# Performance work log

Measured on AMD Instinct MI355X. Metric: run time of the kernel, lower is better.

Reference implementation:

```python
import jax, jax.numpy as jnp
import numpy as np
import math

B, S, D, H = 2, 2048, 512, 8
DK = D // H


def setup_inputs() -> dict:
    key = jax.random.key(0)
    ks = jax.random.split(key, 8)
    scale = 1.0 / math.sqrt(D)
    inp = {
        "query": jax.random.normal(ks[0], (B, S, D), dtype=jnp.float32),
        "key": jax.random.normal(ks[1], (B, S, D), dtype=jnp.float32),
        "value": jax.random.normal(ks[2], (B, S, D), dtype=jnp.float32),
        # causal mask, broadcast over batch and heads; masked_fill where mask == 0
        "mask": jnp.tril(jnp.ones((S, S), dtype=jnp.int32))[None, None, :, :],
        # nn.Linear(d_model, d_model, bias=False) weights, shape [out, in]
        "Wq": jax.random.uniform(ks[3], (D, D), jnp.float32, -scale, scale),
        "Wk": jax.random.uniform(ks[4], (D, D), jnp.float32, -scale, scale),
        "Wv": jax.random.uniform(ks[5], (D, D), jnp.float32, -scale, scale),
        "Wo": jax.random.uniform(ks[6], (D, D), jnp.float32, -scale, scale),
    }
    return inp


def reference(query, key, value, mask, Wq, Wk, Wv, Wo):
    b, s, d = query.shape
    h, dk = H, d // H
    q = query @ Wq.T                      # [B,S,D]
    _k_dead = key @ Wk.T                  # computed then discarded by the repo bug
    v = value @ Wv.T                      # [B,S,D]
    # raw .view() head split (NOT transpose-based) — faithful to the source
    qh = q.reshape(b, h, s, dk)           # [B,H,S,dk]
    kh = qh                               # repo bug: key = query.view(...)
    vh = v.reshape(b, h, s, dk)
    scores = jnp.einsum("bhqd,bhkd->bhqk", qh, kh) / math.sqrt(dk)  # [B,H,S,S]
    scores = jnp.where(mask == 0, jnp.float32(-1e9), scores)
    attn = jax.nn.softmax(scores, axis=-1)  # dropout p=0.0 -> identity
    x = jnp.einsum("bhqk,bhkd->bhqd", attn, vh)  # [B,H,S,dk]
    x = x.transpose(0, 2, 1, 3).reshape(b, s, h * dk)  # [B,S,D]
    return x @ Wo.T
```

## Files before the change

kernel.cpp:

```cpp
#include <hip/hip_runtime.h>


typedef unsigned short u16;
typedef unsigned int   u32;
typedef __attribute__((ext_vector_type(4))) float f32x4;
typedef __attribute__((ext_vector_type(8))) short bf16x8;
typedef __attribute__((ext_vector_type(4))) u16   us4;
typedef __attribute__((ext_vector_type(8))) u16   us8;

#define DEV static __device__ __forceinline__

DEV u16 f2b(float x) {
  union { float f; u32 u; } a; a.f = x;
  u32 u = a.u;
  u += 0x7fffu + ((u >> 16) & 1u);
  return (u16)(u >> 16);
}
DEV float b2f(u16 x) { union { u32 u; float f; } a; a.u = (u32)x << 16; return a.f; }
DEV us4 f4tob(f32x4 v) {
  us4 r; r[0] = f2b(v[0]); r[1] = f2b(v[1]); r[2] = f2b(v[2]); r[3] = f2b(v[3]);
  return r;
}

DEV u32 cvtpk(float lo, float hi) {
  u32 d;
  asm("v_cvt_pk_bf16_f32 %0, %1, %2" : "=v"(d) : "v"(lo), "v"(hi));
  return d;
}
DEV void swap32(u32& a, u32& b) {
  asm("v_permlane32_swap_b32 %0, %1" : "+v"(a), "+v"(b));
}
DEV void swap16(u32& a, u32& b) {
  asm("v_permlane16_swap_b32 %0, %1" : "+v"(a), "+v"(b));
}
DEV void swap32f(float& a, float& b) {
  asm("v_permlane32_swap_b32 %0, %1" : "+v"(a), "+v"(b));
}
DEV void swap16f(float& a, float& b) {
  asm("v_permlane16_swap_b32 %0, %1" : "+v"(a), "+v"(b));
}

DEV void gload16(const u16* g, u16* l) {
  __builtin_amdgcn_global_load_lds(
      (const __attribute__((address_space(1))) void*)(const void*)g,
      (__attribute__((address_space(3))) void*)(void*)l, 16, 0, 0);
}

__global__ __launch_bounds__(256)
void cvt_kernel(const float* __restrict__ q, const float* __restrict__ v,
                const float* __restrict__ wq, const float* __restrict__ wv,
                const float* __restrict__ wo,
                u16* __restrict__ aq, u16* __restrict__ av,
                u16* __restrict__ bq, u16* __restrict__ bv, u16* __restrict__ bo) {
  int cid = blockIdx.x * 256 + threadIdx.x;
  const float* src; u16* dst; int off;
  if      (cid < 262144) { src = q;  dst = aq; off = cid; }
  else if (cid < 524288) { src = v;  dst = av; off = cid - 262144; }
  else if (cid < 557056) { src = wq; dst = bq; off = cid - 524288; }
  else if (cid < 589824) { src = wv; dst = bv; off = cid - 557056; }
  else                   { src = wo; dst = bo; off = cid - 589824; }
  f32x4 a = *reinterpret_cast<const f32x4*>(src + (size_t)off * 8);
  f32x4 b = *reinterpret_cast<const f32x4*>(src + (size_t)off * 8 + 4);
  us4 lo = f4tob(a), hi = f4tob(b);
  us8 o;
  o[0] = lo[0]; o[1] = lo[1]; o[2] = lo[2]; o[3] = lo[3];
  o[4] = hi[0]; o[5] = hi[1]; o[6] = hi[2]; o[7] = hi[3];
  *reinterpret_cast<us8*>(dst + (size_t)off * 8) = o;
}

template<int EPI>
DEV void gemm_fast_body(const u16* __restrict__ A, const u16* __restrict__ Bw,
                        void* __restrict__ outp, int bm, int bn,
                        u16* __restrict__ sA, u16* __restrict__ sB) {
  const int tid  = threadIdx.x;
  const int lane = tid & 63;
  const int w    = tid >> 6;
  const int row0 = bm * 64, col0 = bn * 64;
  const int l16 = lane & 15, lhi = lane >> 4;
  const int wr = (w >> 1) * 32, wc = (w & 1) * 32;

  f32x4 acc[2][2];
#pragma unroll
  for (int mf = 0; mf < 2; ++mf)
#pragma unroll
    for (int nf = 0; nf < 2; ++nf) acc[mf][nf] = (f32x4)0.f;

  auto stage = [&](int buf, int kt) {
#pragma unroll
    for (int i = 0; i < 2; ++i) {
      int u0 = w * 128 + i * 64;
      int u  = u0 + lane;
      int r  = u >> 3;
      int s  = (u & 7) ^ (r & 7);
      gload16(A  + (size_t)(row0 + r) * 512 + kt + s * 8, &sA[buf * 4096 + u0 * 8]);
      gload16(Bw + (size_t)(col0 + r) * 512 + kt + s * 8, &sB[buf * 4096 + u0 * 8]);
    }
  };

  stage(0, 0);
  for (int t = 0; t < 8; ++t) {
    __syncthreads();
    if (t + 1 < 8) stage((t + 1) & 1, (t + 1) * 64);
    const u16* Ka = &sA[(t & 1) * 4096];
    const u16* Kb = &sB[(t & 1) * 4096];
    __builtin_amdgcn_s_setprio(1);
#pragma unroll
    for (int ks = 0; ks < 2; ++ks) {
      bf16x8 af[2], bv[2];
#pragma unroll
      for (int mf = 0; mf < 2; ++mf) {
        int unit = (ks * 4 + lhi) ^ (l16 & 7);
        af[mf] = *reinterpret_cast<const bf16x8*>(&Ka[(wr + mf * 16 + l16) * 64 + unit * 8]);
      }
#pragma unroll
      for (int nf = 0; nf < 2; ++nf) {
        int unit = (ks * 4 + lhi) ^ (l16 & 7);
        bv[nf] = *reinterpret_cast<const bf16x8*>(&Kb[(wc + nf * 16 + l16) * 64 + unit * 8]);
      }
#pragma unroll
      for (int mf = 0; mf < 2; ++mf)
#pragma unroll
        for (int nf = 0; nf < 2; ++nf)
          acc[mf][nf] = __builtin_amdgcn_mfma_f32_16x16x32_bf16(af[mf], bv[nf], acc[mf][nf], 0, 0, 0);
    }
    __builtin_amdgcn_s_setprio(0);
  }

#pragma unroll
  for (int mf = 0; mf < 2; ++mf)
#pragma unroll
    for (int nf = 0; nf < 2; ++nf)
#pragma unroll
      for (int r = 0; r < 4; ++r) {
        int grow = row0 + wr + mf * 16 + lhi * 4 + r;
        int gcol = col0 + wc + nf * 16 + l16;
        float v = acc[mf][nf][r];
        if constexpr (EPI == 0) {
          ((u16*)outp)[(size_t)grow * 512 + gcol] = f2b(v);
        } else if constexpr (EPI == 1) {
          int b = grow >> 11, srow = grow & 2047;
          int h = srow >> 8;
          int ss = ((srow & 255) << 3) + (gcol >> 6);
          int dd = gcol & 63;
          ((u16*)outp)[(((size_t)(b * 8 + h) * 64 + dd) << 11) + ss] = f2b(v);
        } else {
          ((float*)outp)[(size_t)grow * 512 + gcol] = v;
        }
      }
}

__global__ __launch_bounds__(256)
void qv_gemm_kernel(const u16* __restrict__ aq, const u16* __restrict__ av,
                    const u16* __restrict__ wqb, const u16* __restrict__ wvb,
                    u16* __restrict__ qbf, u16* __restrict__ vt) {
  __shared__ u16 sA[2 * 4096];
  __shared__ u16 sB[2 * 4096];
  const int xcd = blockIdx.x & 7;
  const int local = blockIdx.x >> 3;
  const int g = local >> 6, rem = local & 63;
  const int bm = xcd * 8 + (rem >> 3), bn = rem & 7;
  if (g == 0) gemm_fast_body<0>(aq, wqb, qbf, bm, bn, sA, sB);
  else        gemm_fast_body<1>(av, wvb, vt,  bm, bn, sA, sB);
}

__global__ __launch_bounds__(256)
void o_gemm_kernel(const u16* __restrict__ opre, const u16* __restrict__ wob,
                   float* __restrict__ out) {
  __shared__ u16 sA[2 * 4096];
  __shared__ u16 sB[2 * 4096];
  const int xcd = blockIdx.x & 7;
  const int local = blockIdx.x >> 3;
  const int bm = xcd * 8 + (local >> 3), bn = local & 7;
  gemm_fast_body<2>(opre, wob, out, bm, bn, sA, sB);
}

constexpr float SCL = 0.125f * 1.44269504088896340736f;
constexpr int NSPLIT = 4;

__global__ __launch_bounds__(256)
void attn_kernel(const u16* __restrict__ qbf, const u16* __restrict__ vt,
                 u16* __restrict__ opart, float* __restrict__ lsum) {
  __shared__ u16 sK[2][4096];
  __shared__ u16 sV[2][4096];
  const int tid  = threadIdx.x;
  const int lane = tid & 63;
  const int w    = tid >> 6;
  const int xcd  = blockIdx.x & 7;
  const int i    = blockIdx.x >> 3;
  const int qb   = 31 - (i >> 3);
  const int r8   = i & 7;
  const int bh   = 2 * xcd + (r8 >> 2);
  const int split = r8 & 3;
  const int q0 = qb * 64 + w * 16;
  const int l16 = lane & 15, lhi = lane >> 4;

  const u16* Qh = qbf + (size_t)bh * (2048 * 64);
  const u16* Vh = vt  + (size_t)bh * (64 * 2048);

  bf16x8 qf[2];
#pragma unroll
  for (int ks = 0; ks < 2; ++ks) {
    union { bf16x8 v; u32 wd[4]; } qw;
    qw.v = *reinterpret_cast<const bf16x8*>(&Qh[(q0 + l16) * 64 + ks * 32 + lhi * 8]);
#pragma unroll
    for (int j = 0; j < 4; ++j) {
      u32 u = qw.wd[j];
      float lo = b2f((u16)(u & 0xffffu)) * SCL;
      float hi = b2f((u16)(u >> 16)) * SCL;
      qw.wd[j] = cvtpk(lo, hi);
    }
    qf[ks] = qw.v;
  }

  f32x4 Oa[4];
#pragma unroll
  for (int nf = 0; nf < 4; ++nf) Oa[nf] = (f32x4)0.f;
  float rs = 0.f;

  const int ntiles = qb + 1;
  const int base = ntiles >> 2, rem = ntiles & 3;
  const int t0 = split * base + (split < rem ? split : rem);
  const int t1 = t0 + base + (split < rem ? 1 : 0);

  auto stage = [&](int buf, int t) {
    const int kb = t * 64;
#pragma unroll
    for (int j = 0; j < 2; ++j) {
      int u0 = w * 128 + j * 64;
      int u  = u0 + lane;
      int r  = u >> 3;
      int s  = (u & 7) ^ (r & 7);
      gload16(Qh + (size_t)(kb + r) * 64 + s * 8, &sK[buf][u0 * 8]);
      gload16(Vh + (size_t)r * 2048 + kb + s * 8, &sV[buf][u0 * 8]);
    }
  };

  if (t0 < t1) {
    stage(t0 & 1, t0);
    for (int kt = t0; kt < t1; ++kt) {
      __syncthreads();
      if (kt + 1 < t1) stage((kt + 1) & 1, kt + 1);
      const int kb = kt * 64;
      const u16* Kl = sK[kt & 1];
      const u16* Vl = sV[kt & 1];
      bf16x8 kf[8], vf[8];
#pragma unroll
      for (int nf = 0; nf < 4; ++nf)
#pragma unroll
        for (int ks = 0; ks < 2; ++ks) {
          int off = (nf * 16 + l16) * 64 + (((ks * 4 + lhi) ^ (l16 & 7)) * 8);
          kf[nf * 2 + ks] = *reinterpret_cast<const bf16x8*>(&Kl[off]);
          vf[nf * 2 + ks] = *reinterpret_cast<const bf16x8*>(&Vl[off]);
        }
      f32x4 s[4];
#pragma unroll
      for (int nf = 0; nf < 4; ++nf) s[nf] = (f32x4)0.f;
      __builtin_amdgcn_s_setprio(1);
#pragma unroll
      for (int nf = 0; nf < 4; ++nf)
#pragma unroll
        for (int ks = 0; ks < 2; ++ks)
          s[nf] = __builtin_amdgcn_mfma_f32_16x16x32_bf16(kf[nf * 2 + ks], qf[ks], s[nf], 0, 0, 0);
      __builtin_amdgcn_s_setprio(0);
      if (kb + 63 > q0) {
        const int row = q0 + l16;
#pragma unroll
        for (int nf = 0; nf < 4; ++nf)
#pragma unroll
          for (int r = 0; r < 4; ++r) {
            int col = kb + nf * 16 + lhi * 4 + r;
            if (col > row) s[nf][r] = -1e30f;
          }
      }
#pragma unroll
      for (int nf = 0; nf < 4; ++nf)
#pragma unroll
        for (int r = 0; r < 4; ++r) {
          float p = exp2f(s[nf][r]);
          s[nf][r] = p;
          rs += p;
        }
      u32 pk[4][2];
#pragma unroll
      for (int nf = 0; nf < 4; ++nf)
#pragma unroll
        for (int rr = 0; rr < 2; ++rr)
          pk[nf][rr] = cvtpk(s[nf][2 * rr], s[nf][2 * rr + 1]);
      union { u32 wd[4]; bf16x8 v; } pa[2];
#pragma unroll
      for (int ks = 0; ks < 2; ++ks)
#pragma unroll
        for (int rr = 0; rr < 2; ++rr) {
          u32 X = pk[2 * ks][rr], Y = pk[2 * ks + 1][rr];
          swap32(X, Y);
          swap16(X, Y);
          pa[ks].wd[rr]     = X;
          pa[ks].wd[2 + rr] = Y;
        }
      __builtin_amdgcn_s_setprio(1);
#pragma unroll
      for (int nf = 0; nf < 4; ++nf)
#pragma unroll
        for (int ks = 0; ks < 2; ++ks)
          Oa[nf] = __builtin_amdgcn_mfma_f32_16x16x32_bf16(pa[ks].v, vf[nf * 2 + ks], Oa[nf], 0, 0, 0);
      __builtin_amdgcn_s_setprio(0);
    }
  }

  {
    float a = rs, b = rs;
    swap16f(a, b);
    float y = a + b;
    float c = y, d = y;
    swap32f(c, d);
    rs = c + d;
  }

  u16* op = opart + ((size_t)split * 32768 + bh * 2048) * 64;
#pragma unroll
  for (int nf = 0; nf < 4; ++nf)
#pragma unroll
    for (int r = 0; r < 4; ++r) {
      int row = q0 + lhi * 4 + r;
      op[(size_t)row * 64 + nf * 16 + l16] = f2b(Oa[nf][r]);
    }
  if (lane < 16)
    lsum[(size_t)split * 32768 + bh * 2048 + q0 + lane] = rs;
}

__global__ __launch_bounds__(256)
void merge_kernel(const u16* __restrict__ opart, const float* __restrict__ lsum,
                  u16* __restrict__ opre) {
  const int gid = blockIdx.x * 256 + threadIdx.x;
  const int row = gid >> 3;
  const int c   = gid & 7;
  float den = 0.f;
#pragma unroll
  for (int s = 0; s < NSPLIT; ++s) den += lsum[(size_t)s * 32768 + row];
  const float inv = 1.f / den;
  float acc[8];
#pragma unroll
  for (int j = 0; j < 8; ++j) acc[j] = 0.f;
#pragma unroll
  for (int s = 0; s < NSPLIT; ++s) {
    us8 o = *reinterpret_cast<const us8*>(&opart[((size_t)s * 32768 + row) * 64 + c * 8]);
#pragma unroll
    for (int j = 0; j < 8; ++j) acc[j] += b2f(o[j]);
  }
  us8 o;
#pragma unroll
  for (int j = 0; j < 8; ++j) o[j] = f2b(acc[j] * inv);
  const int bh = row >> 11, srow = row & 2047;
  const int b = bh >> 3, h = bh & 7;
  *reinterpret_cast<us8*>(&opre[((size_t)b * 2048 + srow) * 512 + h * 64 + c * 8]) = o;
}

extern "C" void kernel_launch(void* const* d_in, const int* in_sizes, int n_in,
                              void* d_out, int out_size, void* d_ws, size_t ws_size,
                              hipStream_t stream) {
  const float* query = (const float*)d_in[0];
  const float* value = (const float*)d_in[2];
  const float* Wq = (const float*)d_in[4];
  const float* Wv = (const float*)d_in[6];
  const float* Wo = (const float*)d_in[7];

  u16* qbf   = (u16*)d_ws;
  u16* vt    = qbf + 2097152;
  u16* opre  = vt + 2097152;
  u16* opart = opre + 2097152;
  u16* aq    = opart + NSPLIT * 2097152;
  u16* av    = aq + 2097152;
  u16* wqb   = av + 2097152;
  u16* wvb   = wqb + 262144;
  u16* wob   = wvb + 262144;
  float* lsum = (float*)(wob + 262144);
  float* out = (float*)d_out;

  cvt_kernel<<<dim3(2432), dim3(256), 0, stream>>>(query, value, Wq, Wv, Wo,
                                                   aq, av, wqb, wvb, wob);
  qv_gemm_kernel<<<dim3(1024), dim3(256), 0, stream>>>(aq, av, wqb, wvb, qbf, vt);
  attn_kernel<<<dim3(2048), dim3(256), 0, stream>>>(qbf, vt, opart, lsum);
  merge_kernel<<<dim3(1024), dim3(256), 0, stream>>>(opart, lsum, opre);
  o_gemm_kernel<<<dim3(512), dim3(256), 0, stream>>>(opre, wob, out);
}
```

Before: 60.81 us.

## Fuse fp32-to-bf16 activation conversion into QV GEMM and split-merge into O GEMM

The standalone conversion of query/value to bf16 is removed. The QV GEMM now loads fp32 activations into registers, converts them and writes swizzled bf16 tiles to LDS, double-buffered around the MFMA loop. The merge kernel is also folded into the output-projection GEMM, which sums the four split partials, normalizes by the summed lsum and writes the A tile directly. This drops two launches and the bf16 intermediate round-trips. In exchange, A loads become register-staged instead of async global-to-LDS and need extra VALU work per tile.

```diff
diff --git a/kernel.cpp b/kernel.cpp
--- a/kernel.cpp
+++ b/kernel.cpp
@@ -47,18 +47,14 @@
 }
 
 __global__ __launch_bounds__(256)
-void cvt_kernel(const float* __restrict__ q, const float* __restrict__ v,
-                const float* __restrict__ wq, const float* __restrict__ wv,
-                const float* __restrict__ wo,
-                u16* __restrict__ aq, u16* __restrict__ av,
-                u16* __restrict__ bq, u16* __restrict__ bv, u16* __restrict__ bo) {
+void cvtw_kernel(const float* __restrict__ wq, const float* __restrict__ wv,
+                 const float* __restrict__ wo,
+                 u16* __restrict__ bq, u16* __restrict__ bv, u16* __restrict__ bo) {
   int cid = blockIdx.x * 256 + threadIdx.x;
   const float* src; u16* dst; int off;
-  if      (cid < 262144) { src = q;  dst = aq; off = cid; }
-  else if (cid < 524288) { src = v;  dst = av; off = cid - 262144; }
-  else if (cid < 557056) { src = wq; dst = bq; off = cid - 524288; }
-  else if (cid < 589824) { src = wv; dst = bv; off = cid - 557056; }
-  else                   { src = wo; dst = bo; off = cid - 589824; }
+  if      (cid < 32768) { src = wq; dst = bq; off = cid; }
+  else if (cid < 65536) { src = wv; dst = bv; off = cid - 32768; }
+  else                  { src = wo; dst = bo; off = cid - 65536; }
   f32x4 a = *reinterpret_cast<const f32x4*>(src + (size_t)off * 8);
   f32x4 b = *reinterpret_cast<const f32x4*>(src + (size_t)off * 8 + 4);
   us4 lo = f4tob(a), hi = f4tob(b);
@@ -68,64 +64,21 @@
   *reinterpret_cast<us8*>(dst + (size_t)off * 8) = o;
 }
 
+DEV void ds_writeA(u16* sA, int buf, int tid, const u32 w0[8]) {
+  union { u32 wd[4]; us8 v; } o0, o1;
+#pragma unroll
+  for (int j = 0; j < 4; ++j) { o0.wd[j] = w0[j]; o1.wd[j] = w0[4 + j]; }
+  int u0 = 2 * tid;
+  int r  = u0 >> 3;
+  int s0 = (u0 & 7) ^ (r & 7);
+  int s1 = ((u0 + 1) & 7) ^ (r & 7);
+  *reinterpret_cast<us8*>(&sA[buf * 4096 + r * 64 + s0 * 8]) = o0.v;
+  *reinterpret_cast<us8*>(&sA[buf * 4096 + r * 64 + s1 * 8]) = o1.v;
+}
+
 template<int EPI>
-DEV void gemm_fast_body(const u16* __restrict__ A, const u16* __restrict__ Bw,
-                        void* __restrict__ outp, int bm, int bn,
-                        u16* __restrict__ sA, u16* __restrict__ sB) {
-  const int tid  = threadIdx.x;
-  const int lane = tid & 63;
-  const int w    = tid >> 6;
-  const int row0 = bm * 64, col0 = bn * 64;
-  const int l16 = lane & 15, lhi = lane >> 4;
-  const int wr = (w >> 1) * 32, wc = (w & 1) * 32;
-
-  f32x4 acc[2][2];
-#pragma unroll
-  for (int mf = 0; mf < 2; ++mf)
-#pragma unroll
-    for (int nf = 0; nf < 2; ++nf) acc[mf][nf] = (f32x4)0.f;
-
-  auto stage = [&](int buf, int kt) {
-#pragma unroll
-    for (int i = 0; i < 2; ++i) {
-      int u0 = w * 128 + i * 64;
-      int u  = u0 + lane;
-      int r  = u >> 3;
-      int s  = (u & 7) ^ (r & 7);
-      gload16(A  + (size_t)(row0 + r) * 512 + kt + s * 8, &sA[buf * 4096 + u0 * 8]);
-      gload16(Bw + (size_t)(col0 + r) * 512 + kt + s * 8, &sB[buf * 4096 + u0 * 8]);
-    }
-  };
-
-  stage(0, 0);
-  for (int t = 0; t < 8; ++t) {
-    __syncthreads();
-    if (t + 1 < 8) stage((t + 1) & 1, (t + 1) * 64);
-    const u16* Ka = &sA[(t & 1) * 4096];
-    const u16* Kb = &sB[(t & 1) * 4096];
-    __builtin_amdgcn_s_setprio(1);
-#pragma unroll
-    for (int ks = 0; ks < 2; ++ks) {
-      bf16x8 af[2], bv[2];
-#pragma unroll
-      for (int mf = 0; mf < 2; ++mf) {
-        int unit = (ks * 4 + lhi) ^ (l16 & 7);
-        af[mf] = *reinterpret_cast<const bf16x8*>(&Ka[(wr + mf * 16 + l16) * 64 + unit * 8]);
-      }
-#pragma unroll
-      for (int nf = 0; nf < 2; ++nf) {
-        int unit = (ks * 4 + lhi) ^ (l16 & 7);
-        bv[nf] = *reinterpret_cast<const bf16x8*>(&Kb[(wc + nf * 16 + l16) * 64 + unit * 8]);
-      }
-#pragma unroll
-      for (int mf = 0; mf < 2; ++mf)
-#pragma unroll
-        for (int nf = 0; nf < 2; ++nf)
-          acc[mf][nf] = __builtin_amdgcn_mfma_f32_16x16x32_bf16(af[mf], bv[nf], acc[mf][nf], 0, 0, 0);
-    }
-    __builtin_amdgcn_s_setprio(0);
-  }
-
+DEV void gemm_epilogue(void* outp, int row0, int col0, int wr, int wc,
+                       int l16, int lhi, const f32x4 acc[2][2]) {
 #pragma unroll
   for (int mf = 0; mf < 2; ++mf)
 #pragma unroll
@@ -149,8 +102,82 @@
       }
 }
 
+template<int EPI>
+DEV void gemm_f32A_body(const float* __restrict__ Af, const u16* __restrict__ Bw,
+                        void* __restrict__ outp, int bm, int bn,
+                        u16* __restrict__ sA, u16* __restrict__ sB) {
+  const int tid  = threadIdx.x;
+  const int lane = tid & 63;
+  const int w    = tid >> 6;
+  const int row0 = bm * 64, col0 = bn * 64;
+  const int l16 = lane & 15, lhi = lane >> 4;
+  const int wr = (w >> 1) * 32, wc = (w & 1) * 32;
+  const int arow = tid >> 2, acol = (tid & 3) * 16;
+
+  f32x4 acc[2][2];
+#pragma unroll
+  for (int mf = 0; mf < 2; ++mf)
+#pragma unroll
+    for (int nf = 0; nf < 2; ++nf) acc[mf][nf] = (f32x4)0.f;
+
+  f32x4 ar[4];
+  auto loadA = [&](int kt) {
+    const float* src = &Af[(size_t)(row0 + arow) * 512 + kt + acol];
+#pragma unroll
+    for (int j = 0; j < 4; ++j) ar[j] = *reinterpret_cast<const f32x4*>(src + j * 4);
+  };
+  auto writeA = [&](int buf) {
+    u32 wds[8];
+#pragma unroll
+    for (int j = 0; j < 4; ++j) {
+      wds[2 * j]     = cvtpk(ar[j][0], ar[j][1]);
+      wds[2 * j + 1] = cvtpk(ar[j][2], ar[j][3]);
+    }
+    u32 ord[8] = {wds[0], wds[1], wds[2], wds[3], wds[4], wds[5], wds[6], wds[7]};
+    ds_writeA(sA, buf, tid, ord);
+  };
+  auto stageB = [&](int buf, int kt) {
+#pragma unroll
+    for (int i = 0; i < 2; ++i) {
+      int u0 = w * 128 + i * 64;
+      int u  = u0 + lane;
+      int r  = u >> 3;
+      int s  = (u & 7) ^ (r & 7);
+      gload16(Bw + (size_t)(col0 + r) * 512 + kt + s * 8, &sB[buf * 4096 + u0 * 8]);
+    }
+  };
+
+  loadA(0); stageB(0, 0); writeA(0);
+  for (int t = 0; t < 8; ++t) {
+    __syncthreads();
+    if (t + 1 < 8) { stageB((t + 1) & 1, (t + 1) * 64); loadA((t + 1) * 64); }
+    const u16* Ka = &sA[(t & 1) * 4096];
+    const u16* Kb = &sB[(t & 1) * 4096];
+    __builtin_amdgcn_s_setprio(1);
+#pragma unroll
+    for (int ks = 0; ks < 2; ++ks) {
+      bf16x8 af[2], bv[2];
+      int unit = (ks * 4 + lhi) ^ (l16 & 7);
+#pragma unroll
+      for (int mf = 0; mf < 2; ++mf)
+        af[mf] = *reinterpret_cast<const bf16x8*>(&Ka[(wr + mf * 16 + l16) * 64 + unit * 8]);
+#pragma unroll
+      for (int nf = 0; nf < 2; ++nf)
+        bv[nf] = *reinterpret_cast<const bf16x8*>(&Kb[(wc + nf * 16 + l16) * 64 + unit * 8]);
+#pragma unroll
+      for (int mf = 0; mf < 2; ++mf)
+#pragma unroll
+        for (int nf = 0; nf < 2; ++nf)
+          acc[mf][nf] = __builtin_amdgcn_mfma_f32_16x16x32_bf16(af[mf], bv[nf], acc[mf][nf], 0, 0, 0);
+    }
+    __builtin_amdgcn_s_setprio(0);
+    if (t + 1 < 8) writeA((t + 1) & 1);
+  }
+  gemm_epilogue<EPI>(outp, row0, col0, wr, wc, l16, lhi, acc);
+}
+
 __global__ __launch_bounds__(256)
-void qv_gemm_kernel(const u16* __restrict__ aq, const u16* __restrict__ av,
+void qv_gemm_kernel(const float* __restrict__ query, const float* __restrict__ value,
                     const u16* __restrict__ wqb, const u16* __restrict__ wvb,
                     u16* __restrict__ qbf, u16* __restrict__ vt) {
   __shared__ u16 sA[2 * 4096];
@@ -159,23 +186,107 @@
   const int local = blockIdx.x >> 3;
   const int g = local >> 6, rem = local & 63;
   const int bm = xcd * 8 + (rem >> 3), bn = rem & 7;
-  if (g == 0) gemm_fast_body<0>(aq, wqb, qbf, bm, bn, sA, sB);
-  else        gemm_fast_body<1>(av, wvb, vt,  bm, bn, sA, sB);
-}
+  if (g == 0) gemm_f32A_body<0>(query, wqb, qbf, bm, bn, sA, sB);
+  else        gemm_f32A_body<1>(value, wvb, vt,  bm, bn, sA, sB);
+}
+
+constexpr int NSPLIT = 4;
 
 __global__ __launch_bounds__(256)
-void o_gemm_kernel(const u16* __restrict__ opre, const u16* __restrict__ wob,
-                   float* __restrict__ out) {
+void o_gemm_kernel(const u16* __restrict__ opart, const float* __restrict__ lsum,
+                   const u16* __restrict__ wob, float* __restrict__ out) {
   __shared__ u16 sA[2 * 4096];
   __shared__ u16 sB[2 * 4096];
+  const int tid  = threadIdx.x;
+  const int lane = tid & 63;
+  const int w    = tid >> 6;
   const int xcd = blockIdx.x & 7;
   const int local = blockIdx.x >> 3;
   const int bm = xcd * 8 + (local >> 3), bn = local & 7;
-  gemm_fast_body<2>(opre, wob, out, bm, bn, sA, sB);
+  const int row0 = bm * 64, col0 = bn * 64;
+  const int l16 = lane & 15, lhi = lane >> 4;
+  const int wr = (w >> 1) * 32, wc = (w & 1) * 32;
+  const int arow = tid >> 2, acol = (tid & 3) * 16;
+  const int bb = bm >> 5;
+  const int srow = ((bm & 31) << 6) + arow;
+
+  f32x4 acc[2][2];
+#pragma unroll
+  for (int mf = 0; mf < 2; ++mf)
+#pragma unroll
+    for (int nf = 0; nf < 2; ++nf) acc[mf][nf] = (f32x4)0.f;
+
+  us8   po[NSPLIT][2];
+  float dens[NSPLIT];
+  auto loadA = [&](int t) {
+    size_t rb = (size_t)(bb * 8 + t) * 2048 + srow;
+#pragma unroll
+    for (int s = 0; s < NSPLIT; ++s) {
+      dens[s] = lsum[(size_t)s * 32768 + rb];
+      const u16* src = &opart[((size_t)s * 32768 + rb) * 64 + acol];
+      po[s][0] = *reinterpret_cast<const us8*>(src);
+      po[s][1] = *reinterpret_cast<const us8*>(src + 8);
+    }
+  };
+  auto writeA = [&](int buf) {
+    float inv = 1.f / (dens[0] + dens[1] + dens[2] + dens[3]);
+    float a[16];
+#pragma unroll
+    for (int j = 0; j < 8; ++j) {
+      float x0 = 0.f, x1 = 0.f;
+#pragma unroll
+      for (int s = 0; s < NSPLIT; ++s) {
+        x0 += b2f((u16)po[s][0][j]);
+        x1 += b2f((u16)po[s][1][j]);
+      }
+      a[j] = x0 * inv; a[8 + j] = x1 * inv;
+    }
+    u32 ord[8];
+#pragma unroll
+    for (int j = 0; j < 8; ++j) ord[j] = cvtpk(a[2 * j], a[2 * j + 1]);
+    ds_writeA(sA, buf, tid, ord);
+  };
+  auto stageB = [&](int buf, int kt) {
+#pragma unroll
+    for (int i = 0; i < 2; ++i) {
+      int u0 = w * 128 + i * 64;
+      int u  = u0 + lane;
+      int r  = u >> 3;
+      int s  = (u & 7) ^ (r & 7);
+      gload16(wob + (size_t)(col0 + r) * 512 + kt + s * 8, &sB[buf * 4096 + u0 * 8]);
+    }
+  };
+
+  loadA(0); stageB(0, 0); writeA(0);
+  for (int t = 0; t < 8; ++t) {
+    __syncthreads();
+    if (t + 1 < 8) { stageB((t + 1) & 1, (t + 1) * 64); loadA(t + 1); }
+    const u16* Ka = &sA[(t & 1) * 4096];
+    const u16* Kb = &sB[(t & 1) * 4096];
+    __builtin_amdgcn_s_setprio(1);
+#pragma unroll
+    for (int ks = 0; ks < 2; ++ks) {
+      bf16x8 af[2], bv[2];
+      int unit = (ks * 4 + lhi) ^ (l16 & 7);
+#pragma unroll
+      for (int mf = 0; mf < 2; ++mf)
+        af[mf] = *reinterpret_cast<const bf16x8*>(&Ka[(wr + mf * 16 + l16) * 64 + unit * 8]);
+#pragma unroll
+      for (int nf = 0; nf < 2; ++nf)
+        bv[nf] = *reinterpret_cast<const bf16x8*>(&Kb[(wc + nf * 16 + l16) * 64 + unit * 8]);
+#pragma unroll
+      for (int mf = 0; mf < 2; ++mf)
+#pragma unroll
+        for (int nf = 0; nf < 2; ++nf)
+          acc[mf][nf] = __builtin_amdgcn_mfma_f32_16x16x32_bf16(af[mf], bv[nf], acc[mf][nf], 0, 0, 0);
+    }
+    __builtin_amdgcn_s_setprio(0);
+    if (t + 1 < 8) writeA((t + 1) & 1);
+  }
+  gemm_epilogue<2>(out, row0, col0, wr, wc, l16, lhi, acc);
 }
 
 constexpr float SCL = 0.125f * 1.44269504088896340736f;
-constexpr int NSPLIT = 4;
 
 __global__ __launch_bounds__(256)
 void attn_kernel(const u16* __restrict__ qbf, const u16* __restrict__ vt,
@@ -328,33 +439,6 @@
     lsum[(size_t)split * 32768 + bh * 2048 + q0 + lane] = rs;
 }
 
-__global__ __launch_bounds__(256)
-void merge_kernel(const u16* __restrict__ opart, const float* __restrict__ lsum,
-                  u16* __restrict__ opre) {
-  const int gid = blockIdx.x * 256 + threadIdx.x;
-  const int row = gid >> 3;
-  const int c   = gid & 7;
-  float den = 0.f;
-#pragma unroll
-  for (int s = 0; s < NSPLIT; ++s) den += lsum[(size_t)s * 32768 + row];
-  const float inv = 1.f / den;
-  float acc[8];
-#pragma unroll
-  for (int j = 0; j < 8; ++j) acc[j] = 0.f;
-#pragma unroll
-  for (int s = 0; s < NSPLIT; ++s) {
-    us8 o = *reinterpret_cast<const us8*>(&opart[((size_t)s * 32768 + row) * 64 + c * 8]);
-#pragma unroll
-    for (int j = 0; j < 8; ++j) acc[j] += b2f(o[j]);
-  }
-  us8 o;
-#pragma unroll
-  for (int j = 0; j < 8; ++j) o[j] = f2b(acc[j] * inv);
-  const int bh = row >> 11, srow = row & 2047;
-  const int b = bh >> 3, h = bh & 7;
-  *reinterpret_cast<us8*>(&opre[((size_t)b * 2048 + srow) * 512 + h * 64 + c * 8]) = o;
-}
-
 extern "C" void kernel_launch(void* const* d_in, const int* in_sizes, int n_in,
                               void* d_out, int out_size, void* d_ws, size_t ws_size,
                               hipStream_t stream) {
@@ -366,20 +450,15 @@
 
   u16* qbf   = (u16*)d_ws;
   u16* vt    = qbf + 2097152;
-  u16* opre  = vt + 2097152;
-  u16* opart = opre + 2097152;
-  u16* aq    = opart + NSPLIT * 2097152;
-  u16* av    = aq + 2097152;
-  u16* wqb   = av + 2097152;
+  u16* opart = vt + 2097152;
+  u16* wqb   = opart + NSPLIT * 2097152;
   u16* wvb   = wqb + 262144;
   u16* wob   = wvb + 262144;
   float* lsum = (float*)(wob + 262144);
   float* out = (float*)d_out;
 
-  cvt_kernel<<<dim3(2432), dim3(256), 0, stream>>>(query, value, Wq, Wv, Wo,
-                                                   aq, av, wqb, wvb, wob);
-  qv_gemm_kernel<<<dim3(1024), dim3(256), 0, stream>>>(aq, av, wqb, wvb, qbf, vt);
+  cvtw_kernel<<<dim3(384), dim3(256), 0, stream>>>(Wq, Wv, Wo, wqb, wvb, wob);
+  qv_gemm_kernel<<<dim3(1024), dim3(256), 0, stream>>>(query, value, wqb, wvb, qbf, vt);
   attn_kernel<<<dim3(2048), dim3(256), 0, stream>>>(qbf, vt, opart, lsum);
-  merge_kernel<<<dim3(1024), dim3(256), 0, stream>>>(opart, lsum, opre);
-  o_gemm_kernel<<<dim3(512), dim3(256), 0, stream>>>(opre, wob, out);
-}
+  o_gemm_kernel<<<dim3(512), dim3(256), 0, stream>>>(opart, lsum, wob, out);
+}
```

Result: slower. 67.16 us, median of 3 (+10.4%).

## Use 128x128 tiles with triple-buffered pipeline in QV projection GEMM

Applied to the files above, without the earlier changes.

The Q/V projection GEMM moves from 64x64 tiles to 128x128 tiles, so each warp computes a 64x64 sub-tile with 16 MFMA accumulators. The grid shrinks from 1024 to 256 blocks. A three-stage LDS ring with two tiles in flight and explicit vmcnt waits replaces the double buffer. The aim is more data reuse per LDS load and better hiding of global-load latency. The trade-off is more registers and LDS per block, and only 256 blocks, which may leave compute units underused on a 256-CU part.

```diff
diff --git a/kernel.cpp b/kernel.cpp
--- a/kernel.cpp
+++ b/kernel.cpp
@@ -68,13 +68,111 @@
   *reinterpret_cast<us8*>(dst + (size_t)off * 8) = o;
 }
 
-template<int EPI>
-DEV void gemm_fast_body(const u16* __restrict__ A, const u16* __restrict__ Bw,
-                        void* __restrict__ outp, int bm, int bn,
-                        u16* __restrict__ sA, u16* __restrict__ sB) {
+__global__ __launch_bounds__(256)
+void qv_gemm_kernel(const u16* __restrict__ aq, const u16* __restrict__ av,
+                    const u16* __restrict__ wqb, const u16* __restrict__ wvb,
+                    u16* __restrict__ qbf, u16* __restrict__ vt) {
+  __shared__ u16 sA[3][8192];
+  __shared__ u16 sB[3][8192];
   const int tid  = threadIdx.x;
   const int lane = tid & 63;
   const int w    = tid >> 6;
+  const int xcd  = blockIdx.x & 7;
+  const int local = blockIdx.x >> 3;
+  const int g    = local >> 4;
+  const int rem  = local & 15;
+  const int bm = xcd * 4 + (rem >> 2), bn = rem & 3;
+  const u16* A  = g ? av  : aq;
+  const u16* Bw = g ? wvb : wqb;
+  const int row0 = bm * 128, col0 = bn * 128;
+  const int l16 = lane & 15, lhi = lane >> 4;
+  const int wr = (w >> 1) * 64, wc = (w & 1) * 64;
+
+  f32x4 acc[4][4];
+#pragma unroll
+  for (int mf = 0; mf < 4; ++mf)
+#pragma unroll
+    for (int nf = 0; nf < 4; ++nf) acc[mf][nf] = (f32x4)0.f;
+
+  auto stage = [&](int buf, int kt) {
+#pragma unroll
+    for (int i = 0; i < 4; ++i) {
+      int u0 = w * 256 + i * 64;
+      int u  = u0 + lane;
+      int r  = u >> 3;
+      int s  = (u & 7) ^ (r & 7);
+      gload16(A  + (size_t)(row0 + r) * 512 + kt + s * 8, &sA[buf][u0 * 8]);
+      gload16(Bw + (size_t)(col0 + r) * 512 + kt + s * 8, &sB[buf][u0 * 8]);
+    }
+  };
+
+  stage(0, 0);
+  stage(1, 64);
+  int cur = 0;
+  for (int t = 0; t < 8; ++t) {
+    if (t < 7) asm volatile("s_waitcnt vmcnt(8)" ::: "memory");
+    else       asm volatile("s_waitcnt vmcnt(0)" ::: "memory");
+    __builtin_amdgcn_s_barrier();
+    __builtin_amdgcn_sched_barrier(0);
+    if (t + 2 < 8) {
+      int nx = cur + 2; if (nx >= 3) nx -= 3;
+      stage(nx, (t + 2) * 64);
+    }
+    const u16* Ka = sA[cur];
+    const u16* Kb = sB[cur];
+    __builtin_amdgcn_s_setprio(1);
+#pragma unroll
+    for (int ks = 0; ks < 2; ++ks) {
+      bf16x8 af[4], bv[4];
+      int unit = (ks * 4 + lhi) ^ (l16 & 7);
+#pragma unroll
+      for (int mf = 0; mf < 4; ++mf)
+        af[mf] = *reinterpret_cast<const bf16x8*>(&Ka[(wr + mf * 16 + l16) * 64 + unit * 8]);
+#pragma unroll
+      for (int nf = 0; nf < 4; ++nf)
+        bv[nf] = *reinterpret_cast<const bf16x8*>(&Kb[(wc + nf * 16 + l16) * 64 + unit * 8]);
+#pragma unroll
+      for (int mf = 0; mf < 4; ++mf)
+#pragma unroll
+        for (int nf = 0; nf < 4; ++nf)
+          acc[mf][nf] = __builtin_amdgcn_mfma_f32_16x16x32_bf16(af[mf], bv[nf], acc[mf][nf], 0, 0, 0);
+    }
+    __builtin_amdgcn_s_setprio(0);
+    if (++cur == 3) cur = 0;
+  }
+
+#pragma unroll
+  for (int mf = 0; mf < 4; ++mf)
+#pragma unroll
+    for (int nf = 0; nf < 4; ++nf)
+#pragma unroll
+      for (int r = 0; r < 4; ++r) {
+        int grow = row0 + wr + mf * 16 + lhi * 4 + r;
+        int gcol = col0 + wc + nf * 16 + l16;
+        float v = acc[mf][nf][r];
+        if (g == 0) {
+          qbf[(size_t)grow * 512 + gcol] = f2b(v);
+        } else {
+          int b = grow >> 11, srow = grow & 2047;
+          int h = srow >> 8;
+          int ss = ((srow & 255) << 3) + (gcol >> 6);
+          int dd = gcol & 63;
+          vt[(((size_t)(b * 8 + h) * 64 + dd) << 11) + ss] = f2b(v);
+        }
+      }
+}
+
+__global__ __launch_bounds__(256)
+void o_gemm_kernel(const u16* __restrict__ opre, const u16* __restrict__ wob,
+                   float* __restrict__ out) {
+  __shared__ u16 sA[2 * 4096];
+  __shared__ u16 sB[2 * 4096];
+  const int tid  = threadIdx.x;
+  const int lane = tid & 63;
+  const int w    = tid >> 6;
+  const int xcd = blockIdx.x & 7;
+  const int local = blockIdx.x >> 3;
+  const int bm = xcd * 8 + (local >> 3), bn = local & 7;
   const int row0 = bm * 64, col0 = bn * 64;
   const int l16 = lane & 15, lhi = lane >> 4;
   const int wr = (w >> 1) * 32, wc = (w & 1) * 32;
@@ -92,8 +190,8 @@
       int u  = u0 + lane;
       int r  = u >> 3;
       int s  = (u & 7) ^ (r & 7);
-      gload16(A  + (size_t)(row0 + r) * 512 + kt + s * 8, &sA[buf * 4096 + u0 * 8]);
-      gload16(Bw + (size_t)(col0 + r) * 512 + kt + s * 8, &sB[buf * 4096 + u0 * 8]);
+      gload16(opre + (size_t)(row0 + r) * 512 + kt + s * 8, &sA[buf * 4096 + u0 * 8]);
+      gload16(wob  + (size_t)(col0 + r) * 512 + kt + s * 8, &sB[buf * 4096 + u0 * 8]);
     }
   };
 
@@ -107,16 +205,13 @@
 #pragma unroll
     for (int ks = 0; ks < 2; ++ks) {
       bf16x8 af[2], bv[2];
-#pragma unroll
-      for (int mf = 0; mf < 2; ++mf) {
-        int unit = (ks * 4 + lhi) ^ (l16 & 7);
+      int unit = (ks * 4 + lhi) ^ (l16 & 7);
+#pragma unroll
+      for (int mf = 0; mf < 2; ++mf)
         af[mf] = *reinterpret_cast<const bf16x8*>(&Ka[(wr + mf * 16 + l16) * 64 + unit * 8]);
-      }
-#pragma unroll
-      for (int nf = 0; nf < 2; ++nf) {
-        int unit = (ks * 4 + lhi) ^ (l16 & 7);
+#pragma unroll
+      for (int nf = 0; nf < 2; ++nf)
         bv[nf] = *reinterpret_cast<const bf16x8*>(&Kb[(wc + nf * 16 + l16) * 64 + unit * 8]);
-      }
 #pragma unroll
       for (int mf = 0; mf < 2; ++mf)
 #pragma unroll
@@ -134,44 +229,8 @@
       for (int r = 0; r < 4; ++r) {
         int grow = row0 + wr + mf * 16 + lhi * 4 + r;
         int gcol = col0 + wc + nf * 16 + l16;
-        float v = acc[mf][nf][r];
-        if constexpr (EPI == 0) {
-          ((u16*)outp)[(size_t)grow * 512 + gcol] = f2b(v);
-        } else if constexpr (EPI == 1) {
-          int b = grow >> 11, srow = grow & 2047;
-          int h = srow >> 8;
-          int ss = ((srow & 255) << 3) + (gcol >> 6);
-          int dd = gcol & 63;
-          ((u16*)outp)[(((size_t)(b * 8 + h) * 64 + dd) << 11) + ss] = f2b(v);
-        } else {
-          ((float*)outp)[(size_t)grow * 512 + gcol] = v;
-        }
+        out[(size_t)grow * 512 + gcol] = acc[mf][nf][r];
       }
-}
-
-__global__ __launch_bounds__(256)
-void qv_gemm_kernel(const u16* __restrict__ aq, const u16* __restrict__ av,
-                    const u16* __restrict__ wqb, const u16* __restrict__ wvb,
-                    u16* __restrict__ qbf, u16* __restrict__ vt) {
-  __shared__ u16 sA[2 * 4096];
-  __shared__ u16 sB[2 * 4096];
-  const int xcd = blockIdx.x & 7;
-  const int local = blockIdx.x >> 3;
-  const int g = local >> 6, rem = local & 63;
-  const int bm = xcd * 8 + (rem >> 3), bn = rem & 7;
-  if (g == 0) gemm_fast_body<0>(aq, wqb, qbf, bm, bn, sA, sB);
-  else        gemm_fast_body<1>(av, wvb, vt,  bm, bn, sA, sB);
-}
-
-__global__ __launch_bounds__(256)
-void o_gemm_kernel(const u16* __restrict__ opre, const u16* __restrict__ wob,
-                   float* __restrict__ out) {
-  __shared__ u16 sA[2 * 4096];
-  __shared__ u16 sB[2 * 4096];
-  const int xcd = blockIdx.x & 7;
-  const int local = blockIdx.x >> 3;
-  const int bm = xcd * 8 + (local >> 3), bn = local & 7;
-  gemm_fast_body<2>(opre, wob, out, bm, bn, sA, sB);
 }
 
 constexpr float SCL = 0.125f * 1.44269504088896340736f;
@@ -378,7 +437,7 @@
 
   cvt_kernel<<<dim3(2432), dim3(256), 0, stream>>>(query, value, Wq, Wv, Wo,
                                                    aq, av, wqb, wvb, wob);
-  qv_gemm_kernel<<<dim3(1024), dim3(256), 0, stream>>>(aq, av, wqb, wvb, qbf, vt);
+  qv_gemm_kernel<<<dim3(256), dim3(256), 0, stream>>>(aq, av, wqb, wvb, qbf, vt);
   attn_kernel<<<dim3(2048), dim3(256), 0, stream>>>(qbf, vt, opart, lsum);
   merge_kernel<<<dim3(1024), dim3(256), 0, stream>>>(opart, lsum, opre);
   o_gemm_kernel<<<dim3(512), dim3(256), 0, stream>>>(opre, wob, out);
```

Result: slower. 64.56 us (+6.2%).

## Process two 16-row query groups per wave in attention to reuse K/V tiles

Applied to the files above, without the earlier changes.

Each attention block now covers 128 query rows instead of 64, and each wave computes two 16-row groups. Both groups reuse the K and V fragments loaded from shared memory, which halves LDS reads and global K/V staging per query row, and the grid drops from 2048 to 1024 blocks. In exchange, register pressure rises (two sets of accumulators and Q fragments), fewer blocks are available for latency hiding, and causal load balance gets coarser. A small hoist of the swizzle index in the GEMM inner loop is also included.

```diff
diff --git a/kernel.cpp b/kernel.cpp
--- a/kernel.cpp
+++ b/kernel.cpp
@@ -107,16 +107,13 @@
 #pragma unroll
     for (int ks = 0; ks < 2; ++ks) {
       bf16x8 af[2], bv[2];
-#pragma unroll
-      for (int mf = 0; mf < 2; ++mf) {
-        int unit = (ks * 4 + lhi) ^ (l16 & 7);
+      int unit = (ks * 4 + lhi) ^ (l16 & 7);
+#pragma unroll
+      for (int mf = 0; mf < 2; ++mf)
         af[mf] = *reinterpret_cast<const bf16x8*>(&Ka[(wr + mf * 16 + l16) * 64 + unit * 8]);
-      }
-#pragma unroll
-      for (int nf = 0; nf < 2; ++nf) {
-        int unit = (ks * 4 + lhi) ^ (l16 & 7);
+#pragma unroll
+      for (int nf = 0; nf < 2; ++nf)
         bv[nf] = *reinterpret_cast<const bf16x8*>(&Kb[(wc + nf * 16 + l16) * 64 + unit * 8]);
-      }
 #pragma unroll
       for (int mf = 0; mf < 2; ++mf)
 #pragma unroll
@@ -187,37 +184,41 @@
   const int w    = tid >> 6;
   const int xcd  = blockIdx.x & 7;
   const int i    = blockIdx.x >> 3;
-  const int qb   = 31 - (i >> 3);
+  const int qb   = 15 - (i >> 3);
   const int r8   = i & 7;
   const int bh   = 2 * xcd + (r8 >> 2);
   const int split = r8 & 3;
-  const int q0 = qb * 64 + w * 16;
+  const int q0 = qb * 128 + w * 32;
   const int l16 = lane & 15, lhi = lane >> 4;
 
   const u16* Qh = qbf + (size_t)bh * (2048 * 64);
   const u16* Vh = vt  + (size_t)bh * (64 * 2048);
 
-  bf16x8 qf[2];
-#pragma unroll
-  for (int ks = 0; ks < 2; ++ks) {
-    union { bf16x8 v; u32 wd[4]; } qw;
-    qw.v = *reinterpret_cast<const bf16x8*>(&Qh[(q0 + l16) * 64 + ks * 32 + lhi * 8]);
-#pragma unroll
-    for (int j = 0; j < 4; ++j) {
-      u32 u = qw.wd[j];
-      float lo = b2f((u16)(u & 0xffffu)) * SCL;
-      float hi = b2f((u16)(u >> 16)) * SCL;
-      qw.wd[j] = cvtpk(lo, hi);
-    }
-    qf[ks] = qw.v;
-  }
-
-  f32x4 Oa[4];
-#pragma unroll
-  for (int nf = 0; nf < 4; ++nf) Oa[nf] = (f32x4)0.f;
-  float rs = 0.f;
-
-  const int ntiles = qb + 1;
+  bf16x8 qf[2][2];
+#pragma unroll
+  for (int g = 0; g < 2; ++g)
+#pragma unroll
+    for (int ks = 0; ks < 2; ++ks) {
+      union { bf16x8 v; u32 wd[4]; } qw;
+      qw.v = *reinterpret_cast<const bf16x8*>(&Qh[(q0 + g * 16 + l16) * 64 + ks * 32 + lhi * 8]);
+#pragma unroll
+      for (int j = 0; j < 4; ++j) {
+        u32 u = qw.wd[j];
+        float lo = b2f((u16)(u & 0xffffu)) * SCL;
+        float hi = b2f((u16)(u >> 16)) * SCL;
+        qw.wd[j] = cvtpk(lo, hi);
+      }
+      qf[g][ks] = qw.v;
+    }
+
+  f32x4 Oa[2][4];
+#pragma unroll
+  for (int g = 0; g < 2; ++g)
+#pragma unroll
+    for (int nf = 0; nf < 4; ++nf) Oa[g][nf] = (f32x4)0.f;
+  float rs0 = 0.f, rs1 = 0.f;
+
+  const int ntiles = 2 * qb + 2;
   const int base = ntiles >> 2, rem = ntiles & 3;
   const int t0 = split * base + (split < rem ? split : rem);
   const int t1 = t0 + base + (split < rem ? 1 : 0);
@@ -252,80 +253,93 @@
           kf[nf * 2 + ks] = *reinterpret_cast<const bf16x8*>(&Kl[off]);
           vf[nf * 2 + ks] = *reinterpret_cast<const bf16x8*>(&Vl[off]);
         }
-      f32x4 s[4];
-#pragma unroll
-      for (int nf = 0; nf < 4; ++nf) s[nf] = (f32x4)0.f;
-      __builtin_amdgcn_s_setprio(1);
-#pragma unroll
-      for (int nf = 0; nf < 4; ++nf)
+#pragma unroll
+      for (int g = 0; g < 2; ++g) {
+        const int rowbase = q0 + g * 16;
+        f32x4 s[4];
+#pragma unroll
+        for (int nf = 0; nf < 4; ++nf) s[nf] = (f32x4)0.f;
+        __builtin_amdgcn_s_setprio(1);
+#pragma unroll
+        for (int nf = 0; nf < 4; ++nf)
+#pragma unroll
+          for (int ks = 0; ks < 2; ++ks)
+            s[nf] = __builtin_amdgcn_mfma_f32_16x16x32_bf16(kf[nf * 2 + ks], qf[g][ks], s[nf], 0, 0, 0);
+        __builtin_amdgcn_s_setprio(0);
+        if (kb + 63 > rowbase) {
+          const int row = rowbase + l16;
+#pragma unroll
+          for (int nf = 0; nf < 4; ++nf)
+#pragma unroll
+            for (int r = 0; r < 4; ++r) {
+              int col = kb + nf * 16 + lhi * 4 + r;
+              if (col > row) s[nf][r] = -1e30f;
+            }
+        }
+        float rsl = 0.f;
+#pragma unroll
+        for (int nf = 0; nf < 4; ++nf)
+#pragma unroll
+          for (int r = 0; r < 4; ++r) {
+            float p = exp2f(s[nf][r]);
+            s[nf][r] = p;
+            rsl += p;
+          }
+        if (g == 0) rs0 += rsl; else rs1 += rsl;
+        u32 pk[4][2];
+#pragma unroll
+        for (int nf = 0; nf < 4; ++nf)
+#pragma unroll
+          for (int rr = 0; rr < 2; ++rr)
+            pk[nf][rr] = cvtpk(s[nf][2 * rr], s[nf][2 * rr + 1]);
+        union { u32 wd[4]; bf16x8 v; } pa[2];
 #pragma unroll
         for (int ks = 0; ks < 2; ++ks)
-          s[nf] = __builtin_amdgcn_mfma_f32_16x16x32_bf16(kf[nf * 2 + ks], qf[ks], s[nf], 0, 0, 0);
-      __builtin_amdgcn_s_setprio(0);
-      if (kb + 63 > q0) {
-        const int row = q0 + l16;
+#pragma unroll
+          for (int rr = 0; rr < 2; ++rr) {
+            u32 X = pk[2 * ks][rr], Y = pk[2 * ks + 1][rr];
+            swap32(X, Y);
+            swap16(X, Y);
+            pa[ks].wd[rr]     = X;
+            pa[ks].wd[2 + rr] = Y;
+          }
+        __builtin_amdgcn_s_setprio(1);
 #pragma unroll
         for (int nf = 0; nf < 4; ++nf)
 #pragma unroll
-          for (int r = 0; r < 4; ++r) {
-            int col = kb + nf * 16 + lhi * 4 + r;
-            if (col > row) s[nf][r] = -1e30f;
-          }
+          for (int ks = 0; ks < 2; ++ks)
+            Oa[g][nf] = __builtin_amdgcn_mfma_f32_16x16x32_bf16(pa[ks].v, vf[nf * 2 + ks], Oa[g][nf], 0, 0, 0);
+        __builtin_amdgcn_s_setprio(0);
       }
-#pragma unroll
-      for (int nf = 0; nf < 4; ++nf)
-#pragma unroll
-        for (int r = 0; r < 4; ++r) {
-          float p = exp2f(s[nf][r]);
-          s[nf][r] = p;
-          rs += p;
-        }
-      u32 pk[4][2];
-#pragma unroll
-      for (int nf = 0; nf < 4; ++nf)
-#pragma unroll
-        for (int rr = 0; rr < 2; ++rr)
-          pk[nf][rr] = cvtpk(s[nf][2 * rr], s[nf][2 * rr + 1]);
-      union { u32 wd[4]; bf16x8 v; } pa[2];
-#pragma unroll
-      for (int ks = 0; ks < 2; ++ks)
-#pragma unroll
-        for (int rr = 0; rr < 2; ++rr) {
-          u32 X = pk[2 * ks][rr], Y = pk[2 * ks + 1][rr];
-          swap32(X, Y);
-          swap16(X, Y);
-          pa[ks].wd[rr]     = X;
-          pa[ks].wd[2 + rr] = Y;
-        }
-      __builtin_amdgcn_s_setprio(1);
-#pragma unroll
-      for (int nf = 0; nf < 4; ++nf)
-#pragma unroll
-        for (int ks = 0; ks < 2; ++ks)
-          Oa[nf] = __builtin_amdgcn_mfma_f32_16x16x32_bf16(pa[ks].v, vf[nf * 2 + ks], Oa[nf], 0, 0, 0);
-      __builtin_amdgcn_s_setprio(0);
-    }
-  }
-
-  {
-    float a = rs, b = rs;
+    }
+  }
+
+#pragma unroll
+  for (int g = 0; g < 2; ++g) {
+    float rsv = g == 0 ? rs0 : rs1;
+    float a = rsv, b = rsv;
     swap16f(a, b);
     float y = a + b;
     float c = y, d = y;
     swap32f(c, d);
-    rs = c + d;
+    rsv = c + d;
+    if (g == 0) rs0 = rsv; else rs1 = rsv;
   }
 
   u16* op = opart + ((size_t)split * 32768 + bh * 2048) * 64;
 #pragma unroll
-  for (int nf = 0; nf < 4; ++nf)
-#pragma unroll
-    for (int r = 0; r < 4; ++r) {
-      int row = q0 + lhi * 4 + r;
-      op[(size_t)row * 64 + nf * 16 + l16] = f2b(Oa[nf][r]);
-    }
-  if (lane < 16)
-    lsum[(size_t)split * 32768 + bh * 2048 + q0 + lane] = rs;
+  for (int g = 0; g < 2; ++g)
+#pragma unroll
+    for (int nf = 0; nf < 4; ++nf)
+#pragma unroll
+      for (int r = 0; r < 4; ++r) {
+        int row = q0 + g * 16 + lhi * 4 + r;
+        op[(size_t)row * 64 + nf * 16 + l16] = f2b(Oa[g][nf][r]);
+      }
+  if (lane < 16) {
+    lsum[(size_t)split * 32768 + bh * 2048 + q0 + lane]      = rs0;
+    lsum[(size_t)split * 32768 + bh * 2048 + q0 + 16 + lane] = rs1;
+  }
 }
 
 __global__ __launch_bounds__(256)
@@ -379,7 +393,7 @@
   cvt_kernel<<<dim3(2432), dim3(256), 0, stream>>>(query, value, Wq, Wv, Wo,
                                                    aq, av, wqb, wvb, wob);
   qv_gemm_kernel<<<dim3(1024), dim3(256), 0, stream>>>(aq, av, wqb, wvb, qbf, vt);
-  attn_kernel<<<dim3(2048), dim3(256), 0, stream>>>(qbf, vt, opart, lsum);
+  attn_kernel<<<dim3(1024), dim3(256), 0, stream>>>(qbf, vt, opart, lsum);
   merge_kernel<<<dim3(1024), dim3(256), 0, stream>>>(opart, lsum, opre);
   o_gemm_kernel<<<dim3(512), dim3(256), 0, stream>>>(opre, wob, out);
 }
```

New measurement: 64.75 us. 1.06x slower.
